# Kernel tuning notes

Hardware: AMD Instinct MI355X
Metric: run time of the kernel (lower is better)

## Reference

```python
import jax, jax.numpy as jnp
import numpy as np
from jax import lax

KH = KW = 3
STRIDE = 1
PAD = 1
DIL = 1
DG = 1  # deformable groups


def setup_inputs() -> dict:
    key = jax.random.key(0)
    k1, k2, k3 = jax.random.split(key, 3)
    B, Cin, H, W = 4, 64, 128, 128
    Cout = 64
    x = jax.random.normal(k1, (B, Cin, H, W), jnp.float32)
    # main conv weight ~ uniform(-1/sqrt(Cin*kh*kw), ...) scale
    weight = jax.random.normal(k2, (Cout, Cin, KH, KW), jnp.float32) * 0.04
    bias = jnp.zeros((Cout,), jnp.float32)
    # offset/mask conv: small weights so offsets stay near the regular grid
    offset_w = jax.random.normal(k3, (DG * 3 * KH * KW, Cin, KH, KW), jnp.float32) * 0.01
    offset_b = jnp.zeros((DG * 3 * KH * KW,), jnp.float32)
    return dict(x=x, weight=weight, bias=bias, offset_w=offset_w, offset_b=offset_b)


def _conv2d(x, w, b):
    out = lax.conv_general_dilated(
        x, w, window_strides=(STRIDE, STRIDE), padding=[(PAD, PAD), (PAD, PAD)],
        rhs_dilation=(DIL, DIL), dimension_numbers=('NCHW', 'OIHW', 'NCHW'))
    return out + b[None, :, None, None]


def _dcn_forward(x, weight, bias, offset_w, offset_b):
    B, Cin, H, W = x.shape
    Cout = weight.shape[0]
    K = KH * KW
    # offset / mask branch (ordinary conv)
    om = _conv2d(x, offset_w, offset_b)            # [B, 3*DG*K, Ho, Wo]
    Ho, Wo = om.shape[2], om.shape[3]
    o1, o2, m = jnp.split(om, 3, axis=1)           # chunk into dy, dx, mask
    dy = o1.reshape(B, DG, K, Ho, Wo)
    dx = o2.reshape(B, DG, K, Ho, Wo)
    mask = jax.nn.sigmoid(m).reshape(B, DG, K, Ho, Wo)
    # regular grid sample positions per kernel tap
    ki = jnp.arange(KH)
    kj = jnp.arange(KW)
    base_h = (jnp.arange(Ho) * STRIDE - PAD)[None, :] + (ki * DIL)[:, None]   # [KH, Ho]
    base_w = (jnp.arange(Wo) * STRIDE - PAD)[None, :] + (kj * DIL)[:, None]   # [KW, Wo]
    base_h = jnp.broadcast_to(base_h[:, None, :, None], (KH, KW, Ho, Wo)).reshape(K, Ho, Wo)
    base_w = jnp.broadcast_to(base_w[None, :, None, :], (KH, KW, Ho, Wo)).reshape(K, Ho, Wo)
    h = base_h[None, None].astype(dy.dtype) + dy   # [B, DG, K, Ho, Wo] float
    w = base_w[None, None].astype(dx.dtype) + dx
    h0 = jnp.floor(h)
    w0 = jnp.floor(w)
    lh = h - h0
    lw = w - w0
    h0i = h0.astype(jnp.int32)
    w0i = w0.astype(jnp.int32)
    Cg = Cin // DG
    xg = x.reshape(B, DG, Cg, H * W)

    def gather(hi, wi):
        # zero-padded bilinear corner gather, shared across the group's channels
        valid = (hi >= 0) & (hi < H) & (wi >= 0) & (wi < W)
        idx = jnp.clip(hi, 0, H - 1) * W + jnp.clip(wi, 0, W - 1)        # [B,DG,K,Ho,Wo]
        idxf = jnp.broadcast_to(idx.reshape(B, DG, 1, K * Ho * Wo), (B, DG, Cg, K * Ho * Wo))
        v = jnp.take_along_axis(xg, idxf, axis=3).reshape(B, DG, Cg, K, Ho, Wo)
        return v * valid[:, :, None].astype(v.dtype)

    wgt = lambda a, b_: (a * b_)[:, :, None]       # -> [B,DG,1,K,Ho,Wo]
    val = (wgt(1 - lh, 1 - lw) * gather(h0i, w0i)
           + wgt(1 - lh, lw) * gather(h0i, w0i + 1)
           + wgt(lh, 1 - lw) * gather(h0i + 1, w0i)
           + wgt(lh, lw) * gather(h0i + 1, w0i + 1))
    cols = val * mask[:, :, None]                  # modulated columns [B,DG,Cg,K,Ho,Wo]
    wk = weight.reshape(Cout, DG, Cg, K)
    out = jnp.einsum('bgckhw,ogck->bohw', cols, wk) + bias[None, :, None, None]
    return out


def reference(x, weight, bias, offset_w, offset_b):
    return _dcn_forward(x, weight, bias, offset_w, offset_b)
```

## Files before the change

kernel.cpp:

```cpp
#include <hip/hip_runtime.h>
#include <hip/hip_fp16.h>

#define B_   4
#define CIN  64
#define HH   128
#define WW   128
#define COUT 64
#define HW   (HH * WW)
#define KK   9

typedef float    f32x4 __attribute__((ext_vector_type(4)));
typedef _Float16 f16x8 __attribute__((ext_vector_type(8)));

union U4 {
    uint4     q;
    uint32_t  u[4];
    __half2   h2[4];
    f16x8     v;
};

#define MFMA16(a, b, c) __builtin_amdgcn_mfma_f32_16x16x32_f16((a).v, (b).v, (c), 0, 0, 0)

__global__ __launch_bounds__(256)
void prep_kernel(const float* __restrict__ x,
                 const float* __restrict__ w,
                 const float* __restrict__ ow,
                 __half* __restrict__ xh,
                 __half* __restrict__ wpack,
                 __half* __restrict__ wop) {
    if (blockIdx.x < 2048) {
        int cg  = blockIdx.x >> 8;
        int pix = (blockIdx.x & 255) * 256 + threadIdx.x;
        int b = pix >> 14, hw = pix & (HW - 1);
        const float* xp = x + (size_t)b * CIN * HW + (size_t)cg * 8 * HW + hw;
        uint32_t u[4];
#pragma unroll
        for (int q = 0; q < 4; ++q) {
            __half2 h = __floats2half2_rn(xp[(size_t)(2 * q) * HW],
                                          xp[(size_t)(2 * q + 1) * HW]);
            u[q] = *(uint32_t*)&h;
        }
        *(uint4*)(xh + (size_t)pix * CIN + cg * 8) = *(const uint4*)u;
    } else {
        int i = (blockIdx.x - 2048) * 256 + threadIdx.x;
        if (i < 36864) {
            int j = i & 7, l = (i >> 3) & 63, s = i >> 9;
            int t = s >> 2;
            int rr = t * 32 + ((l >> 4) << 3) + j;
            int c = rr & 63, k = rr >> 6;
            int o = (s & 3) * 16 + (l & 15);
            wpack[i] = __float2half(w[(o * CIN + c) * KK + k]);
        } else {
            int i2 = i - 36864;
            int j = i2 & 7, l = (i2 >> 3) & 63, s = i2 >> 9;
            int t = s >> 1;
            int rr = t * 32 + ((l >> 4) << 3) + j;
            int c = rr & 63, k = rr >> 6;
            int o = (s & 1) * 16 + (l & 15);
            wop[i2] = __float2half((o < 27) ? ow[(o * CIN + c) * KK + k] : 0.f);
        }
    }
}

__global__ __launch_bounds__(512, 2)
void dcn_fused_kernel(const __half* __restrict__ xh,
                      const __half* __restrict__ wop,
                      const float* __restrict__ ob,
                      const __half* __restrict__ wpack,
                      const float* __restrict__ bias,
                      float* __restrict__ out) {
    int bid0 = blockIdx.x;
    int bid  = (bid0 & 7) * 32 + (bid0 >> 3);
    int b = bid >> 6, rp = bid & 63;
    int ho0 = rp * 2;
    int tid = threadIdx.x;
    int w = tid >> 6, l = tid & 63;
    int p = l & 15, grp = l >> 4, grp16 = grp << 4;
    int r = w >> 2, q = w & 3;
    int ho = ho0 + r;
    int wo0 = q * 32;

    __shared__ __align__(16) char  xs[131072];
    __shared__ __half lomh[8][27][34];

    const char* xb = (const char*)xh + (size_t)b * HW * CIN * 2;

#pragma unroll
    for (int it = 0; it < 16; ++it) {
        int idx = it * 512 + tid;
        int rr = idx >> 10, c16 = idx & 1023;
        int col = c16 >> 3, sub = c16 & 7;
        int srow = min(max(ho0 - 3 + rr, 0), HH - 1);
        uint4 v = *(const uint4*)(xb + ((size_t)srow << 14) + (col << 7) + (sub << 4));
        *(uint4*)(xs + (((rr << 14) + (col << 7) + (sub << 4)) ^ ((col & 7) << 4))) = v;
    }
    __syncthreads();

    {
        const uint4* wpo = (const uint4*)wop + l;
        int aad[2][9], asw[2][9];
        uint32_t avm[2][9];
#pragma unroll
        for (int m = 0; m < 2; ++m)
#pragma unroll
        for (int k = 0; k < 9; ++k) {
            int ki = k / 3, kj = k % 3;
            int hh = ho + ki - 1;
            int cr = wo0 + m * 16 + p + kj - 1;
            bool v = ((unsigned)hh < (unsigned)HH) && ((unsigned)cr < (unsigned)WW);
            int slot = r + ki + 2;
            int cc = min(max(cr, 0), WW - 1);
            aad[m][k] = (slot << 14) + (cc << 7) + grp16;
            asw[m][k] = (cc & 7) << 4;
            avm[m][k] = v ? 0xffffffffu : 0u;
        }
        f32x4 oacc[2][2] = {};
#pragma unroll
        for (int t = 0; t < 18; ++t) {
            int k = t >> 1, half = t & 1;
            U4 a0, a1;
            a0.q = *(const uint4*)(xs + ((aad[0][k] + (half << 6)) ^ asw[0][k]));
            a1.q = *(const uint4*)(xs + ((aad[1][k] + (half << 6)) ^ asw[1][k]));
#pragma unroll
            for (int i = 0; i < 4; ++i) { a0.u[i] &= avm[0][k]; a1.u[i] &= avm[1][k]; }
            U4 b0, b1;
            b0.q = wpo[(t * 2 + 0) * 64];
            b1.q = wpo[(t * 2 + 1) * 64];
            oacc[0][0] = MFMA16(a0, b0, oacc[0][0]);
            oacc[0][1] = MFMA16(a0, b1, oacc[0][1]);
            oacc[1][0] = MFMA16(a1, b0, oacc[1][0]);
            oacc[1][1] = MFMA16(a1, b1, oacc[1][1]);
        }
#pragma unroll
        for (int m = 0; m < 2; ++m)
#pragma unroll
        for (int nt = 0; nt < 2; ++nt) {
            int oc = nt * 16 + (l & 15);
            if (oc < 27) {
                float bv = ob[oc];
#pragma unroll
                for (int i = 0; i < 4; ++i) {
                    float vv = oacc[m][nt][i] + bv;
                    if (oc >= 18) vv = 1.f / (1.f + __expf(-vv));
                    lomh[w][oc][m * 16 + grp * 4 + i] = __float2half(vv);
                }
            }
        }
    }

    f32x4 acc[2][4] = {};
    const uint4* wpm = (const uint4*)wpack + l;

#pragma unroll
    for (int k = 0; k < 9; ++k) {
        int ch0[2], ch1[2], cw0[2], cw1[2];
        __half2 hwA[2], hwB[2], hwC[2], hwD[2];
        int okall = 1;
#pragma unroll
        for (int m = 0; m < 2; ++m) {
            int px = m * 16 + p;
            float dy = __half2float(lomh[w][k][px]);
            float dx = __half2float(lomh[w][9 + k][px]);
            float mk = __half2float(lomh[w][18 + k][px]);
            float hf = (float)(ho - 1 + k / 3) + dy;
            float wf = (float)(wo0 + px - 1 + k % 3) + dx;
            float h0f = floorf(hf), w0f = floorf(wf);
            float lh = hf - h0f, lw = wf - w0f;
            int h0 = (int)h0f, w0i = (int)w0f;
            int h1 = h0 + 1, w1i = w0i + 1;
            bool vh0 = (unsigned)h0 < (unsigned)HH, vh1 = (unsigned)h1 < (unsigned)HH;
            bool vw0 = (unsigned)w0i < (unsigned)WW, vw1 = (unsigned)w1i < (unsigned)WW;
            int c0 = min(max(h0, 0), HH - 1), c1 = min(max(h1, 0), HH - 1);
            int d0 = min(max(w0i, 0), WW - 1), d1 = min(max(w1i, 0), WW - 1);
            ch0[m] = c0; ch1[m] = c1; cw0[m] = d0; cw1[m] = d1;
            float fA = (vh0 && vw0) ? (1.f - lh) * (1.f - lw) * mk : 0.f;
            float fB = (vh0 && vw1) ? (1.f - lh) * lw * mk : 0.f;
            float fC = (vh1 && vw0) ? lh * (1.f - lw) * mk : 0.f;
            float fD = (vh1 && vw1) ? lh * lw * mk : 0.f;
            hwA[m] = __float2half2_rn(fA); hwB[m] = __float2half2_rn(fB);
            hwC[m] = __float2half2_rn(fC); hwD[m] = __float2half2_rn(fD);
            int s0 = c0 + 3 - ho0, s1 = c1 + 3 - ho0;
            okall &= (int)((unsigned)s0 <= 7u) & (int)((unsigned)s1 <= 7u);
        }
        int okw = __all(okall);

#pragma unroll
        for (int half = 0; half < 2; ++half) {
            int t = 2 * k + half;
            int hb = (half << 6) + grp16;
            U4 bf0, bf1, bf2, bf3;
            bf0.q = wpm[(t * 4 + 0) * 64];
            bf1.q = wpm[(t * 4 + 1) * 64];
            bf2.q = wpm[(t * 4 + 2) * 64];
            bf3.q = wpm[(t * 4 + 3) * 64];
            U4 a[2];
            if (okw) {
#pragma unroll
                for (int m = 0; m < 2; ++m) {
                    int s0 = ch0[m] + 3 - ho0, s1 = ch1[m] + 3 - ho0;
                    U4 u0, u1, u2, u3;
                    u0.q = *(const uint4*)(xs + (((s0 << 14) + (cw0[m] << 7) + hb) ^ ((cw0[m] & 7) << 4)));
                    u1.q = *(const uint4*)(xs + (((s0 << 14) + (cw1[m] << 7) + hb) ^ ((cw1[m] & 7) << 4)));
                    u2.q = *(const uint4*)(xs + (((s1 << 14) + (cw0[m] << 7) + hb) ^ ((cw0[m] & 7) << 4)));
                    u3.q = *(const uint4*)(xs + (((s1 << 14) + (cw1[m] << 7) + hb) ^ ((cw1[m] & 7) << 4)));
#pragma unroll
                    for (int i = 0; i < 4; ++i)
                        a[m].h2[i] = __hfma2(hwD[m], u3.h2[i],
                                     __hfma2(hwC[m], u2.h2[i],
                                     __hfma2(hwB[m], u1.h2[i],
                                     __hmul2(hwA[m], u0.h2[i]))));
                }
            } else {
#pragma unroll
                for (int m = 0; m < 2; ++m) {
                    U4 u0, u1, u2, u3;
                    u0.q = *(const uint4*)(xb + ((size_t)ch0[m] << 14) + (cw0[m] << 7) + hb);
                    u1.q = *(const uint4*)(xb + ((size_t)ch0[m] << 14) + (cw1[m] << 7) + hb);
                    u2.q = *(const uint4*)(xb + ((size_t)ch1[m] << 14) + (cw0[m] << 7) + hb);
                    u3.q = *(const uint4*)(xb + ((size_t)ch1[m] << 14) + (cw1[m] << 7) + hb);
#pragma unroll
                    for (int i = 0; i < 4; ++i)
                        a[m].h2[i] = __hfma2(hwD[m], u3.h2[i],
                                     __hfma2(hwC[m], u2.h2[i],
                                     __hfma2(hwB[m], u1.h2[i],
                                     __hmul2(hwA[m], u0.h2[i]))));
                }
            }
            acc[0][0] = MFMA16(a[0], bf0, acc[0][0]);
            acc[0][1] = MFMA16(a[0], bf1, acc[0][1]);
            acc[0][2] = MFMA16(a[0], bf2, acc[0][2]);
            acc[0][3] = MFMA16(a[0], bf3, acc[0][3]);
            acc[1][0] = MFMA16(a[1], bf0, acc[1][0]);
            acc[1][1] = MFMA16(a[1], bf1, acc[1][1]);
            acc[1][2] = MFMA16(a[1], bf2, acc[1][2]);
            acc[1][3] = MFMA16(a[1], bf3, acc[1][3]);
        }
    }

#pragma unroll
    for (int m = 0; m < 2; ++m)
#pragma unroll
    for (int nt = 0; nt < 4; ++nt) {
        int oc = nt * 16 + (l & 15);
        float bv = bias[oc];
        f32x4 s;
#pragma unroll
        for (int i = 0; i < 4; ++i) s[i] = acc[m][nt][i] + bv;
        *(f32x4*)(out + ((size_t)(b * COUT + oc)) * HW + ho * WW + wo0 + m * 16 + grp * 4) = s;
    }
}

extern "C" void kernel_launch(void* const* d_in, const int* in_sizes, int n_in,
                              void* d_out, int out_size, void* d_ws, size_t ws_size,
                              hipStream_t stream) {
    const float* x    = (const float*)d_in[0];
    const float* wgt  = (const float*)d_in[1];
    const float* bias = (const float*)d_in[2];
    const float* ow   = (const float*)d_in[3];
    const float* ob   = (const float*)d_in[4];
    float* out = (float*)d_out;

    char* ws = (char*)d_ws;
    __half* wpack = (__half*)ws;
    __half* wop   = (__half*)(ws + 73728);
    __half* xh    = (__half*)(ws + 73728 + 36864);

    prep_kernel<<<2048 + 216, 256, 0, stream>>>(x, wgt, ow, xh, wpack, wop);
    dcn_fused_kernel<<<B_ * HH / 2, 512, 0, stream>>>(xh, wop, ob, wpack, bias, out);
}
```

Measured before the change: 100.0 us.

## Fuse fp32-to-fp16 NHWC conversion of x into the DCN kernel's shared-memory load

Drops the separate prep pass that converted x to an fp16 channels-last workspace buffer. The fused kernel now reads fp32 NCHW x directly, converts to half and writes the swizzled shared-memory tile. The out-of-tile fallback path gathers eight strided fp32 channel values per corner instead of one 16-byte load. This saves a full write and re-read of the converted tensor, but makes each staging load narrower and the fallback gather much more scattered.

```diff
diff --git a/kernel.cpp b/kernel.cpp
--- a/kernel.cpp
+++ b/kernel.cpp
@@ -22,48 +22,31 @@
 #define MFMA16(a, b, c) __builtin_amdgcn_mfma_f32_16x16x32_f16((a).v, (b).v, (c), 0, 0, 0)
 
 __global__ __launch_bounds__(256)
-void prep_kernel(const float* __restrict__ x,
-                 const float* __restrict__ w,
+void prep_kernel(const float* __restrict__ w,
                  const float* __restrict__ ow,
-                 __half* __restrict__ xh,
                  __half* __restrict__ wpack,
                  __half* __restrict__ wop) {
-    if (blockIdx.x < 2048) {
-        int cg  = blockIdx.x >> 8;
-        int pix = (blockIdx.x & 255) * 256 + threadIdx.x;
-        int b = pix >> 14, hw = pix & (HW - 1);
-        const float* xp = x + (size_t)b * CIN * HW + (size_t)cg * 8 * HW + hw;
-        uint32_t u[4];
-#pragma unroll
-        for (int q = 0; q < 4; ++q) {
-            __half2 h = __floats2half2_rn(xp[(size_t)(2 * q) * HW],
-                                          xp[(size_t)(2 * q + 1) * HW]);
-            u[q] = *(uint32_t*)&h;
-        }
-        *(uint4*)(xh + (size_t)pix * CIN + cg * 8) = *(const uint4*)u;
+    int i = blockIdx.x * 256 + threadIdx.x;
+    if (i < 36864) {
+        int j = i & 7, l = (i >> 3) & 63, s = i >> 9;
+        int t = s >> 2;
+        int rr = t * 32 + ((l >> 4) << 3) + j;
+        int c = rr & 63, k = rr >> 6;
+        int o = (s & 3) * 16 + (l & 15);
+        wpack[i] = __float2half(w[(o * CIN + c) * KK + k]);
     } else {
-        int i = (blockIdx.x - 2048) * 256 + threadIdx.x;
-        if (i < 36864) {
-            int j = i & 7, l = (i >> 3) & 63, s = i >> 9;
-            int t = s >> 2;
-            int rr = t * 32 + ((l >> 4) << 3) + j;
-            int c = rr & 63, k = rr >> 6;
-            int o = (s & 3) * 16 + (l & 15);
-            wpack[i] = __float2half(w[(o * CIN + c) * KK + k]);
-        } else {
-            int i2 = i - 36864;
-            int j = i2 & 7, l = (i2 >> 3) & 63, s = i2 >> 9;
-            int t = s >> 1;
-            int rr = t * 32 + ((l >> 4) << 3) + j;
-            int c = rr & 63, k = rr >> 6;
-            int o = (s & 1) * 16 + (l & 15);
-            wop[i2] = __float2half((o < 27) ? ow[(o * CIN + c) * KK + k] : 0.f);
-        }
+        int i2 = i - 36864;
+        int j = i2 & 7, l = (i2 >> 3) & 63, s = i2 >> 9;
+        int t = s >> 1;
+        int rr = t * 32 + ((l >> 4) << 3) + j;
+        int c = rr & 63, k = rr >> 6;
+        int o = (s & 1) * 16 + (l & 15);
+        wop[i2] = __float2half((o < 27) ? ow[(o * CIN + c) * KK + k] : 0.f);
     }
 }
 
 __global__ __launch_bounds__(512, 2)
-void dcn_fused_kernel(const __half* __restrict__ xh,
+void dcn_fused_kernel(const float* __restrict__ x,
                       const __half* __restrict__ wop,
                       const float* __restrict__ ob,
                       const __half* __restrict__ wpack,
@@ -83,16 +66,24 @@
     __shared__ __align__(16) char  xs[131072];
     __shared__ __half lomh[8][27][34];
 
-    const char* xb = (const char*)xh + (size_t)b * HW * CIN * 2;
+    const float* xbF = x + (size_t)b * CIN * HW;
 
 #pragma unroll
     for (int it = 0; it < 16; ++it) {
-        int idx = it * 512 + tid;
-        int rr = idx >> 10, c16 = idx & 1023;
-        int col = c16 >> 3, sub = c16 & 7;
+        int cg  = it & 7;
+        int pix = (it >> 3) * 512 + tid;
+        int rr = pix >> 7, col = pix & 127;
         int srow = min(max(ho0 - 3 + rr, 0), HH - 1);
-        uint4 v = *(const uint4*)(xb + ((size_t)srow << 14) + (col << 7) + (sub << 4));
-        *(uint4*)(xs + (((rr << 14) + (col << 7) + (sub << 4)) ^ ((col & 7) << 4))) = v;
+        const float* xp = xbF + (size_t)(cg * 8) * HW + srow * WW + col;
+        uint32_t u[4];
+#pragma unroll
+        for (int j = 0; j < 4; ++j) {
+            __half2 h = __floats2half2_rn(xp[(size_t)(2 * j) * HW],
+                                          xp[(size_t)(2 * j + 1) * HW]);
+            u[j] = *(uint32_t*)&h;
+        }
+        *(uint4*)(xs + (((rr << 14) + (col << 7) + (cg << 4)) ^ ((col & 7) << 4)))
+            = *(const uint4*)u;
     }
     __syncthreads();
 
@@ -211,13 +202,22 @@
                                      __hmul2(hwA[m], u0.h2[i]))));
                 }
             } else {
+                const float* cbase = xbF + (size_t)(32 * half + grp * 8) * HW;
 #pragma unroll
                 for (int m = 0; m < 2; ++m) {
                     U4 u0, u1, u2, u3;
-                    u0.q = *(const uint4*)(xb + ((size_t)ch0[m] << 14) + (cw0[m] << 7) + hb);
-                    u1.q = *(const uint4*)(xb + ((size_t)ch0[m] << 14) + (cw1[m] << 7) + hb);
-                    u2.q = *(const uint4*)(xb + ((size_t)ch1[m] << 14) + (cw0[m] << 7) + hb);
-                    u3.q = *(const uint4*)(xb + ((size_t)ch1[m] << 14) + (cw1[m] << 7) + hb);
+#pragma unroll
+                    for (int j = 0; j < 4; ++j) {
+                        const float* p0 = cbase + (size_t)(2 * j) * HW;
+                        const float* p1 = cbase + (size_t)(2 * j + 1) * HW;
+                        int i00 = ch0[m] * WW + cw0[m], i01 = ch0[m] * WW + cw1[m];
+                        int i10 = ch1[m] * WW + cw0[m], i11 = ch1[m] * WW + cw1[m];
+                        __half2 h;
+                        h = __floats2half2_rn(p0[i00], p1[i00]); u0.u[j] = *(uint32_t*)&h;
+                        h = __floats2half2_rn(p0[i01], p1[i01]); u1.u[j] = *(uint32_t*)&h;
+                        h = __floats2half2_rn(p0[i10], p1[i10]); u2.u[j] = *(uint32_t*)&h;
+                        h = __floats2half2_rn(p0[i11], p1[i11]); u3.u[j] = *(uint32_t*)&h;
+                    }
 #pragma unroll
                     for (int i = 0; i < 4; ++i)
                         a[m].h2[i] = __hfma2(hwD[m], u3.h2[i],
@@ -263,8 +263,7 @@
     char* ws = (char*)d_ws;
     __half* wpack = (__half*)ws;
     __half* wop   = (__half*)(ws + 73728);
-    __half* xh    = (__half*)(ws + 73728 + 36864);
-
-    prep_kernel<<<2048 + 216, 256, 0, stream>>>(x, wgt, ow, xh, wpack, wop);
-    dcn_fused_kernel<<<B_ * HH / 2, 512, 0, stream>>>(xh, wop, ob, wpack, bias, out);
+
+    prep_kernel<<<216, 256, 0, stream>>>(wgt, ow, wpack, wop);
+    dcn_fused_kernel<<<B_ * HH / 2, 512, 0, stream>>>(x, wop, ob, wpack, bias, out);
 }
```

After: 96.32 us. -3.7%, faster.
